# Performance work log

Measured on AMD Instinct MI355X. Metric: run time of the kernel, lower is better.

Reference implementation:

```python
import jax, jax.numpy as jnp
import numpy as np

EPS = 1e-08


def setup_inputs() -> dict:
    key = jax.random.key(0)
    B, D = 8192, 512
    student_output = jax.random.normal(key, (B, D), dtype=jnp.float32)
    return {"student_output": student_output}


def reference(student_output) -> jnp.ndarray:
    # F.normalize(p=2, dim=-1, eps=EPS): x / max(||x||, eps)
    norm = jnp.linalg.norm(student_output, axis=-1, keepdims=True)
    x = student_output / jnp.maximum(norm, EPS)

    n = x.shape[0]
    # Pairwise inner products; mask the diagonal with -1 (self-match)
    dots = jnp.matmul(x, x.T)  # [B, B]
    idx = jnp.arange(n)
    dots = dots.at[idx, idx].set(-1.0)
    I = jnp.argmax(dots, axis=1)  # nearest neighbor index per row

    # torch.nn.PairwiseDistance(2, eps): ||x1 - x2 + eps||_2
    diff = x - x[I] + EPS
    distances = jnp.linalg.norm(diff, axis=-1)  # [B]
    loss = -jnp.mean(jnp.log(distances + EPS))
    return loss
```

## Files before the change

kernel.cpp:

```cpp
#include <hip/hip_runtime.h>
#include <hip/hip_bf16.h>
#include <math.h>

#define D_DIM 512
#define TM    128
#define TN    256
#define BK    128

typedef int i32x4 __attribute__((ext_vector_type(4)));
typedef unsigned long long u64;


__device__ inline u64 shfl_xor_u64(u64 x, int m) {
    int lo = __shfl_xor((int)(unsigned)(x & 0xFFFFFFFFull), m, 64);
    int hi = __shfl_xor((int)(unsigned)(x >> 32), m, 64);
    return ((u64)(unsigned)hi << 32) | (u64)(unsigned)lo;
}

__device__ inline void async16(unsigned char* lds, const unsigned char* g) {
    __builtin_amdgcn_global_load_lds(
        (const __attribute__((address_space(1))) void*)g,
        (__attribute__((address_space(3))) void*)lds,
        16, 0, 0);
}


__global__ __launch_bounds__(256) void normalize_rows(
        const float* __restrict__ in, unsigned char* __restrict__ xb,
        float* __restrict__ inv_norm, u64* __restrict__ best,
        float* __restrict__ acc, int* __restrict__ cnt) {
    const int row  = blockIdx.x * 4 + (threadIdx.x >> 6);
    const int lane = threadIdx.x & 63;
    if (blockIdx.x == 0 && threadIdx.x == 0) { acc[0] = 0.f; cnt[0] = 0; }
    const float4* rp = (const float4*)(in + (size_t)row * D_DIM) + lane * 2;
    float4 a = rp[0], b = rp[1];
    float s = a.x*a.x + a.y*a.y + a.z*a.z + a.w*a.w
            + b.x*b.x + b.y*b.y + b.z*b.z + b.w*b.w;
    #pragma unroll
    for (int m = 1; m <= 32; m <<= 1) s += __shfl_xor(s, m, 64);
    float inv = 1.0f / fmaxf(sqrtf(s), 1e-8f);
    if (lane == 0) {
        inv_norm[row] = inv;
        best[row] = 0ull;
    }
    float sc = inv * 127.0f;
    int q0 = __float2int_rn(a.x*sc), q1 = __float2int_rn(a.y*sc);
    int q2 = __float2int_rn(a.z*sc), q3 = __float2int_rn(a.w*sc);
    int q4 = __float2int_rn(b.x*sc), q5 = __float2int_rn(b.y*sc);
    int q6 = __float2int_rn(b.z*sc), q7 = __float2int_rn(b.w*sc);
    int lo = (q0 & 255) | ((q1 & 255) << 8) | ((q2 & 255) << 16) | ((q3 & 255) << 24);
    int hi = (q4 & 255) | ((q5 & 255) << 8) | ((q6 & 255) << 16) | ((q7 & 255) << 24);
    ((int2*)(xb + (size_t)row * D_DIM))[lane] = make_int2(lo, hi);
}


__global__ __launch_bounds__(256, 2) void gemm_argmax(
        const unsigned char* __restrict__ X, u64* __restrict__ best) {
    __shared__ unsigned char As[TM * BK];
    __shared__ unsigned char Bs[TN * BK];
    __shared__ u64 rmerge[TM * 2];
    __shared__ u64 cmerge[TN * 2];

    int l = blockIdx.x;
    int q = (int)(sqrtf((float)l / 16.0f + 0.25f) - 0.5f);
    while (16 * (q + 1) * (q + 2) <= l) ++q;
    while (16 * q * (q + 1) > l) --q;
    int rrem = l - 16 * q * (q + 1);
    int cw   = 8 * (q + 1);
    int c    = rrem / cw;
    int bi   = rrem - c * cw;
    int bj   = 4 * q + c;
    if (bi > 2 * bj + 1) return;
    const int m0 = bi * TM;
    const int n0 = bj * TN;

    const int t    = threadIdx.x;
    const int lane = t & 63;
    const int w    = t >> 6;
    const int wm   = w >> 1, wn = w & 1;
    const int qr   = lane & 15;
    const int quad = lane >> 4;

    const int rS   = t >> 3;
    const int gSrc = ((t & 7) ^ ((t >> 3) & 7)) * 16;
    const unsigned char* gA = X + (size_t)(m0 + rS) * D_DIM + gSrc;
    const unsigned char* gB = X + (size_t)(n0 + rS) * D_DIM + gSrc;

    i32x4 accm[4][8];
    #pragma unroll
    for (int mi = 0; mi < 4; mi++)
        #pragma unroll
        for (int ni = 0; ni < 8; ni++)
            accm[mi][ni] = (i32x4){0, 0, 0, 0};

    for (int k0 = 0; k0 < D_DIM; k0 += BK) {
        #pragma unroll
        for (int j = 0; j < 4; j++)
            async16(As + j * 4096 + t * 16, gA + (size_t)(j * 32) * D_DIM + k0);
        #pragma unroll
        for (int j = 0; j < 8; j++)
            async16(Bs + j * 4096 + t * 16, gB + (size_t)(j * 32) * D_DIM + k0);
        __syncthreads();

        #pragma unroll
        for (int ks = 0; ks < 2; ks++) {
            i32x4 av[4], bv[8];
            #pragma unroll
            for (int mi = 0; mi < 4; mi++) {
                int r   = wm * 64 + mi * 16 + qr;
                int pos = (ks * 4 + quad) ^ (r & 7);
                av[mi] = *(const i32x4*)(As + r * BK + pos * 16);
            }
            #pragma unroll
            for (int ni = 0; ni < 8; ni++) {
                int r   = wn * 128 + ni * 16 + qr;
                int pos = (ks * 4 + quad) ^ (r & 7);
                bv[ni] = *(const i32x4*)(Bs + r * BK + pos * 16);
            }
            #pragma unroll
            for (int mi = 0; mi < 4; mi++)
                #pragma unroll
                for (int ni = 0; ni < 8; ni++)
                    accm[mi][ni] = __builtin_amdgcn_mfma_i32_16x16x64_i8(
                        av[mi], bv[ni], accm[mi][ni], 0, 0, 0);
        }
        __syncthreads();
    }

    const int colg_base = n0 + wn * 128 + qr;
    #pragma unroll
    for (int mi = 0; mi < 4; mi++) {
        #pragma unroll
        for (int r = 0; r < 4; r++) {
            const int rowl = wm * 64 + mi * 16 + quad * 4 + r;
            const int rowg = m0 + rowl;
            u64 key = 0ull;
            #pragma unroll
            for (int ni = 0; ni < 8; ni++) {
                int colg = colg_base + ni * 16;
                if (colg == rowg) continue;
                unsigned bd = (unsigned)accm[mi][ni][r] + 0x80000000u;
                u64 k = ((u64)bd << 32) | (u64)(0xFFFFFFFFu - (unsigned)colg);
                key = key > k ? key : k;
            }
            #pragma unroll
            for (int m = 1; m <= 8; m <<= 1) {
                u64 o = shfl_xor_u64(key, m);
                key = key > o ? key : o;
            }
            if (qr == 0) rmerge[rowl * 2 + wn] = key;
        }
    }

    #pragma unroll
    for (int ni = 0; ni < 8; ni++) {
        const int colg = colg_base + ni * 16;
        u64 key = 0ull;
        #pragma unroll
        for (int mi = 0; mi < 4; mi++) {
            #pragma unroll
            for (int r = 0; r < 4; r++) {
                int rowg = m0 + wm * 64 + mi * 16 + quad * 4 + r;
                if (rowg == colg) continue;
                unsigned bd = (unsigned)accm[mi][ni][r] + 0x80000000u;
                u64 k = ((u64)bd << 32) | (u64)(0xFFFFFFFFu - (unsigned)rowg);
                key = key > k ? key : k;
            }
        }
        u64 o = shfl_xor_u64(key, 16); key = key > o ? key : o;
        o     = shfl_xor_u64(key, 32); key = key > o ? key : o;
        if (quad == 0) cmerge[(wn * 128 + ni * 16 + qr) * 2 + wm] = key;
    }
    __syncthreads();
    if (t < TM) {
        u64 a = rmerge[t * 2], b = rmerge[t * 2 + 1];
        u64 k = a > b ? a : b;
        atomicMax(&best[m0 + t], k);
    }
    {
        u64 ca = cmerge[t * 2], cb = cmerge[t * 2 + 1];
        u64 ck = ca > cb ? ca : cb;
        atomicMax(&best[n0 + t], ck);
    }
}


__global__ __launch_bounds__(256) void neighbor_reduce(
        const float* __restrict__ in, const float* __restrict__ inv_norm,
        const u64* __restrict__ best, float* __restrict__ acc,
        int* __restrict__ cnt, float* __restrict__ out, int B) {
    const int wave = threadIdx.x >> 6;
    const int lane = threadIdx.x & 63;
    float lsum = 0.f;
    #pragma unroll
    for (int rr = 0; rr < 8; rr++) {
        const int row = blockIdx.x * 32 + wave * 8 + rr;
        u64 k   = best[row];
        int nbr = (int)(0xFFFFFFFFu - (unsigned)(k & 0xFFFFFFFFull));
        float ir  = inv_norm[row];
        float inb = inv_norm[nbr];
        const float4* rp = (const float4*)(in + (size_t)row * D_DIM) + lane * 2;
        const float4* np = (const float4*)(in + (size_t)nbr * D_DIM) + lane * 2;
        float4 r0 = rp[0], r1 = rp[1], q0 = np[0], q1 = np[1];
        float d0 = r0.x*ir - q0.x*inb + 1e-8f, d1 = r0.y*ir - q0.y*inb + 1e-8f;
        float d2 = r0.z*ir - q0.z*inb + 1e-8f, d3 = r0.w*ir - q0.w*inb + 1e-8f;
        float d4 = r1.x*ir - q1.x*inb + 1e-8f, d5 = r1.y*ir - q1.y*inb + 1e-8f;
        float d6 = r1.z*ir - q1.z*inb + 1e-8f, d7 = r1.w*ir - q1.w*inb + 1e-8f;
        float s = d0*d0 + d1*d1 + d2*d2 + d3*d3 + d4*d4 + d5*d5 + d6*d6 + d7*d7;
        #pragma unroll
        for (int m = 1; m <= 32; m <<= 1) s += __shfl_xor(s, m, 64);
        if (lane == 0) lsum += logf(sqrtf(s) + 1e-8f);
    }
    __shared__ float sb[4];
    if (lane == 0) sb[wave] = lsum;
    __syncthreads();
    if (threadIdx.x == 0) {
        float partial = sb[0] + sb[1] + sb[2] + sb[3];
        atomicAdd(acc, partial);
        __threadfence();
        int done = atomicAdd(cnt, 1);
        if (done == gridDim.x - 1) {
            __threadfence();
            float tot = atomicAdd(acc, 0.0f);
            out[0] = -tot / (float)B;
        }
    }
}


extern "C" void kernel_launch(void* const* d_in, const int* in_sizes, int n_in,
                              void* d_out, int out_size, void* d_ws, size_t ws_size,
                              hipStream_t stream) {
    const float* in = (const float*)d_in[0];
    const int B = in_sizes[0] / D_DIM;
    const int nblk = 16 * 8 * 9;

    char* w = (char*)d_ws;
    unsigned char* xb = (unsigned char*)w;
    float* invn = (float*)(w + (size_t)B * D_DIM);
    u64*   best = (u64*)(w + (size_t)B * D_DIM + (size_t)B * 4);
    float* acc  = (float*)(w + (size_t)B * D_DIM + (size_t)B * 4 + (size_t)B * 8);
    int*   cnt  = (int*)(acc + 1);
    float* out  = (float*)d_out;

    normalize_rows<<<B / 4, 256, 0, stream>>>(in, xb, invn, best, acc, cnt);
    gemm_argmax<<<nblk, 256, 0, stream>>>(xb, best);
    neighbor_reduce<<<B / 32, 256, 0, stream>>>(in, invn, best, acc, cnt, out, B);
}
```

Baseline: 116.4 us.

## Fuse neighbor distance reduction into GEMM kernel via per-band completion counters

Removes the separate neighbor_reduce launch by appending 64 extra blocks to the gemm_argmax grid. Each extra block spins on a per-row-band counter until every GEMM tile touching that band has finished its atomicMax updates, then computes the distances, logs and partial sum, with a global counter producing the final loss. This is meant to save a kernel launch and overlap the tail reduction with the remaining GEMM tiles. It relies on the spinning blocks not starving the GEMM tiles of CU slots and on block scheduling order, so it risks deadlock or stalls if the band blocks are dispatched before the work they wait on.

```diff
diff --git a/kernel.cpp b/kernel.cpp
--- a/kernel.cpp
+++ b/kernel.cpp
@@ -6,6 +6,8 @@
 #define TM    128
 #define TN    256
 #define BK    128
+#define NMAIN 1152
+#define NBAND 64
 
 typedef int i32x4 __attribute__((ext_vector_type(4)));
 typedef unsigned long long u64;
@@ -28,10 +30,15 @@
 __global__ __launch_bounds__(256) void normalize_rows(
         const float* __restrict__ in, unsigned char* __restrict__ xb,
         float* __restrict__ inv_norm, u64* __restrict__ best,
-        float* __restrict__ acc, int* __restrict__ cnt) {
+        float* __restrict__ acc, int* __restrict__ gcnt,
+        int* __restrict__ bandcnt) {
     const int row  = blockIdx.x * 4 + (threadIdx.x >> 6);
     const int lane = threadIdx.x & 63;
-    if (blockIdx.x == 0 && threadIdx.x == 0) { acc[0] = 0.f; cnt[0] = 0; }
+    if (blockIdx.x == 0) {
+        if (threadIdx.x < NBAND) bandcnt[threadIdx.x] = 0;
+        if (threadIdx.x == NBAND)     acc[0]  = 0.f;
+        if (threadIdx.x == NBAND + 1) gcnt[0] = 0;
+    }
     const float4* rp = (const float4*)(in + (size_t)row * D_DIM) + lane * 2;
     float4 a = rp[0], b = rp[1];
     float s = a.x*a.x + a.y*a.y + a.z*a.z + a.w*a.w
@@ -55,13 +62,66 @@
 
 
 __global__ __launch_bounds__(256, 2) void gemm_argmax(
-        const unsigned char* __restrict__ X, u64* __restrict__ best) {
+        const unsigned char* __restrict__ X, u64* __restrict__ best,
+        const float* __restrict__ in, const float* __restrict__ inv_norm,
+        float* __restrict__ acc, int* __restrict__ gcnt,
+        int* __restrict__ bandcnt, float* __restrict__ out, int B) {
     __shared__ unsigned char As[TM * BK];
     __shared__ unsigned char Bs[TN * BK];
     __shared__ u64 rmerge[TM * 2];
     __shared__ u64 cmerge[TN * 2];
 
-    int l = blockIdx.x;
+    const int l    = blockIdx.x;
+    const int t    = threadIdx.x;
+    const int lane = t & 63;
+    const int w    = t >> 6;
+
+    if (l >= NMAIN) {
+        const int band = l - NMAIN;
+        const int expected = 34 + (band >> 1);
+        __shared__ int ready;
+        if (t == 0) {
+            while (atomicAdd(&bandcnt[band], 0) < expected)
+                __builtin_amdgcn_s_sleep(32);
+            ready = 1;
+        }
+        __syncthreads();
+        (void)ready;
+
+        float lsum = 0.f;
+        for (int i = 0; i < 32; i++) {
+            const int row = band * TM + w * 32 + i;
+            u64 k   = atomicMax(&best[row], 0ull);
+            int nbr = (int)(0xFFFFFFFFu - (unsigned)(k & 0xFFFFFFFFull));
+            float ir  = inv_norm[row];
+            float inb = inv_norm[nbr];
+            const float4* rp = (const float4*)(in + (size_t)row * D_DIM) + lane * 2;
+            const float4* np = (const float4*)(in + (size_t)nbr * D_DIM) + lane * 2;
+            float4 r0 = rp[0], r1 = rp[1], q0 = np[0], q1 = np[1];
+            float d0 = r0.x*ir - q0.x*inb + 1e-8f, d1 = r0.y*ir - q0.y*inb + 1e-8f;
+            float d2 = r0.z*ir - q0.z*inb + 1e-8f, d3 = r0.w*ir - q0.w*inb + 1e-8f;
+            float d4 = r1.x*ir - q1.x*inb + 1e-8f, d5 = r1.y*ir - q1.y*inb + 1e-8f;
+            float d6 = r1.z*ir - q1.z*inb + 1e-8f, d7 = r1.w*ir - q1.w*inb + 1e-8f;
+            float s = d0*d0 + d1*d1 + d2*d2 + d3*d3 + d4*d4 + d5*d5 + d6*d6 + d7*d7;
+            #pragma unroll
+            for (int m = 1; m <= 32; m <<= 1) s += __shfl_xor(s, m, 64);
+            if (lane == 0) lsum += logf(sqrtf(s) + 1e-8f);
+        }
+        __shared__ float sbf[4];
+        if (lane == 0) sbf[w] = lsum;
+        __syncthreads();
+        if (t == 0) atomicAdd(acc, sbf[0] + sbf[1] + sbf[2] + sbf[3]);
+        __syncthreads();
+        if (t == 0) {
+            int d = atomicAdd(gcnt, 1);
+            if (d == NBAND - 1) {
+                float tot = atomicAdd(acc, 0.0f);
+                out[0] = -tot / (float)B;
+            }
+        }
+        return;
+    }
+
     int q = (int)(sqrtf((float)l / 16.0f + 0.25f) - 0.5f);
     while (16 * (q + 1) * (q + 2) <= l) ++q;
     while (16 * q * (q + 1) > l) --q;
@@ -74,9 +134,6 @@
     const int m0 = bi * TM;
     const int n0 = bj * TN;
 
-    const int t    = threadIdx.x;
-    const int lane = t & 63;
-    const int w    = t >> 6;
     const int wm   = w >> 1, wn = w & 1;
     const int qr   = lane & 15;
     const int quad = lane >> 4;
@@ -182,49 +239,11 @@
         u64 ck = ca > cb ? ca : cb;
         atomicMax(&best[n0 + t], ck);
     }
-}
-
-
-__global__ __launch_bounds__(256) void neighbor_reduce(
-        const float* __restrict__ in, const float* __restrict__ inv_norm,
-        const u64* __restrict__ best, float* __restrict__ acc,
-        int* __restrict__ cnt, float* __restrict__ out, int B) {
-    const int wave = threadIdx.x >> 6;
-    const int lane = threadIdx.x & 63;
-    float lsum = 0.f;
-    #pragma unroll
-    for (int rr = 0; rr < 8; rr++) {
-        const int row = blockIdx.x * 32 + wave * 8 + rr;
-        u64 k   = best[row];
-        int nbr = (int)(0xFFFFFFFFu - (unsigned)(k & 0xFFFFFFFFull));
-        float ir  = inv_norm[row];
-        float inb = inv_norm[nbr];
-        const float4* rp = (const float4*)(in + (size_t)row * D_DIM) + lane * 2;
-        const float4* np = (const float4*)(in + (size_t)nbr * D_DIM) + lane * 2;
-        float4 r0 = rp[0], r1 = rp[1], q0 = np[0], q1 = np[1];
-        float d0 = r0.x*ir - q0.x*inb + 1e-8f, d1 = r0.y*ir - q0.y*inb + 1e-8f;
-        float d2 = r0.z*ir - q0.z*inb + 1e-8f, d3 = r0.w*ir - q0.w*inb + 1e-8f;
-        float d4 = r1.x*ir - q1.x*inb + 1e-8f, d5 = r1.y*ir - q1.y*inb + 1e-8f;
-        float d6 = r1.z*ir - q1.z*inb + 1e-8f, d7 = r1.w*ir - q1.w*inb + 1e-8f;
-        float s = d0*d0 + d1*d1 + d2*d2 + d3*d3 + d4*d4 + d5*d5 + d6*d6 + d7*d7;
-        #pragma unroll
-        for (int m = 1; m <= 32; m <<= 1) s += __shfl_xor(s, m, 64);
-        if (lane == 0) lsum += logf(sqrtf(s) + 1e-8f);
-    }
-    __shared__ float sb[4];
-    if (lane == 0) sb[wave] = lsum;
+
     __syncthreads();
-    if (threadIdx.x == 0) {
-        float partial = sb[0] + sb[1] + sb[2] + sb[3];
-        atomicAdd(acc, partial);
-        __threadfence();
-        int done = atomicAdd(cnt, 1);
-        if (done == gridDim.x - 1) {
-            __threadfence();
-            float tot = atomicAdd(acc, 0.0f);
-            out[0] = -tot / (float)B;
-        }
-    }
+    if (t == 0) atomicAdd(&bandcnt[bi], 1);
+    if (t == 1) atomicAdd(&bandcnt[2 * bj], 1);
+    if (t == 2) atomicAdd(&bandcnt[2 * bj + 1], 1);
 }
 
 
@@ -233,17 +252,17 @@
                               hipStream_t stream) {
     const float* in = (const float*)d_in[0];
     const int B = in_sizes[0] / D_DIM;
-    const int nblk = 16 * 8 * 9;
 
     char* w = (char*)d_ws;
     unsigned char* xb = (unsigned char*)w;
-    float* invn = (float*)(w + (size_t)B * D_DIM);
-    u64*   best = (u64*)(w + (size_t)B * D_DIM + (size_t)B * 4);
-    float* acc  = (float*)(w + (size_t)B * D_DIM + (size_t)B * 4 + (size_t)B * 8);
-    int*   cnt  = (int*)(acc + 1);
-    float* out  = (float*)d_out;
-
-    normalize_rows<<<B / 4, 256, 0, stream>>>(in, xb, invn, best, acc, cnt);
-    gemm_argmax<<<nblk, 256, 0, stream>>>(xb, best);
-    neighbor_reduce<<<B / 32, 256, 0, stream>>>(in, invn, best, acc, cnt, out, B);
-}
+    float* invn    = (float*)(w + (size_t)B * D_DIM);
+    u64*   best    = (u64*)(w + (size_t)B * D_DIM + (size_t)B * 4);
+    float* acc     = (float*)(w + (size_t)B * D_DIM + (size_t)B * 4 + (size_t)B * 8);
+    int*   gcnt    = (int*)(acc + 1);
+    int*   bandcnt = (int*)(acc + 2);
+    float* out     = (float*)d_out;
+
+    normalize_rows<<<B / 4, 256, 0, stream>>>(in, xb, invn, best, acc, gcnt, bandcnt);
+    gemm_argmax<<<NMAIN + NBAND, 256, 0, stream>>>(xb, best, in, invn,
+                                                   acc, gcnt, bandcnt, out, B);
+}
```

Result: slower. 140.0 us (+20.2%).
